# Kernel tuning notes

Measured on AMD Instinct MI355X. Metric: run time of the kernel, lower is better.

Reference implementation:

```python
import jax, jax.numpy as jnp
import numpy as np


def _ccl(x, w, b):
    # FFT-domain circular conv: rfft2 -> complex multiply + sum over c_in -> irfft2 + bias
    H, W = x.shape[-2], x.shape[-1]
    xf = jnp.fft.rfft2(x)                 # [B, Ci, H, Wf] complex
    wf = jnp.fft.rfft2(w, s=(H, W))       # [Co, Ci, H, Wf] complex
    hf = jnp.einsum('bihw,oihw->bohw', xf, wf)
    return jnp.fft.irfft2(hf, s=(H, W)) + b[:, None, None]


def _maxpool(x, ph, pw):
    B, C, H, W = x.shape
    return x.reshape(B, C, H // ph, ph, W // pw, pw).max(axis=(3, 5))


def _upsample_zero(x, sh, sw):
    B, C, H, W = x.shape
    y = jnp.zeros((B, C, H * sh, W * sw), dtype=x.dtype)
    return y.at[:, :, ::sh, ::sw].set(x)


def setup_inputs() -> dict:
    key = jax.random.key(0)
    ks = jax.random.split(key, 11)
    inp = {"x": jax.random.normal(ks[0], (16, 2, 64, 256), dtype=jnp.float32)}
    specs = [  # (c_out, c_in, kh, kw)
        (50, 1, 3, 7), (50, 50, 3, 7), (50, 50, 3, 5), (50, 50, 3, 7), (1, 50, 3, 7)]
    for i, (co, ci, kh, kw) in enumerate(specs):
        K = float(np.sqrt(1.0 / (ci * kh * kw)))
        inp[f"w{i+1}"] = (2 * jax.random.uniform(ks[2 * i + 1], (co, ci, kh, kw), dtype=jnp.float32) - 1) * K
        inp[f"b{i+1}"] = (2 * jax.random.uniform(ks[2 * i + 2], (co,), dtype=jnp.float32) - 1) * K
    return inp


def reference(x, w1, b1, w2, b2, w3, b3, w4, b4, w5, b5):
    H, W = x.shape[-2], x.shape[-1]
    h = x.reshape(-1, 1, H, W)                       # [2B, 1, 64, 256]
    h = jax.nn.relu(_maxpool(_ccl(h, w1, b1), 2, 4))  # [2B, 50, 32, 64]
    h = jax.nn.relu(_maxpool(_ccl(h, w2, b2), 2, 4))  # [2B, 50, 16, 16]
    h = h.reshape(-1, 2, h.shape[-3], h.shape[-2], h.shape[-1])
    h = h[:, 0] + h[:, 1].mean(axis=(-1, -2))[..., None, None]  # [B, 50, 16, 16]
    h = jax.nn.relu(_ccl(_upsample_zero(h, 2, 4), w3, b3))       # [B, 50, 32, 64]
    h = jax.nn.relu(_ccl(_upsample_zero(h, 2, 4), w4, b4))       # [B, 50, 64, 256]
    h = jax.nn.sigmoid(_ccl(h, w5, b5))                          # [B, 1, 64, 256]
    return h.squeeze(1)
```

## Files before the change

### kernel.cpp

```cpp
#include <hip/hip_runtime.h>
#include <math.h>

__global__ void kprep(const float* __restrict__ w2, const float* __restrict__ w3,
                      const float* __restrict__ w4, float* __restrict__ w2t,
                      float* __restrict__ w3t, float* __restrict__ w4t) {
  int i = blockIdx.x * 256 + threadIdx.x;
  if (i < 52500) {
    int co = i % 50, r = i / 50;
    w2t[i] = w2[co * 1050 + r];
    w4t[i] = w4[co * 1050 + r];
  } else {
    int j = i - 52500;
    if (j < 37500) {
      int co = j % 50, r = j / 50;
      w3t[j] = w3[co * 750 + r];
    }
  }
}

__global__ __launch_bounds__(256) void k1(const float* __restrict__ x,
                                          const float* __restrict__ w1,
                                          const float* __restrict__ b1,
                                          float* __restrict__ a1) {
  int b = blockIdx.z;
  int pr0 = blockIdx.x * 4;
  int co0 = blockIdx.y * 10;
  int ty = threadIdx.x >> 6;
  int pc = threadIdx.x & 63;
  int pr = pr0 + ty;
  const float* xb = x + b * (64 * 256);
  float xw[4][10];
#pragma unroll
  for (int r = 0; r < 4; ++r) {
    int row = (2 * pr - 2 + r) & 63;
#pragma unroll
    for (int c = 0; c < 10; ++c) {
      int col = (4 * pc - 6 + c) & 255;
      xw[r][c] = xb[row * 256 + col];
    }
  }
#pragma unroll
  for (int cq = 0; cq < 10; ++cq) {
    int co = co0 + cq;
    const float* wp = w1 + co * 21;
    float m = -1e30f;
#pragma unroll
    for (int iy = 0; iy < 2; ++iy) {
#pragma unroll
      for (int jx = 0; jx < 4; ++jx) {
        float s = 0.f;
#pragma unroll
        for (int di = 0; di < 3; ++di)
#pragma unroll
          for (int dj = 0; dj < 7; ++dj)
            s = fmaf(xw[iy + 2 - di][jx + 6 - dj], wp[di * 7 + dj], s);
        m = fmaxf(m, s);
      }
    }
    float v = fmaxf(m + b1[co], 0.f);
    a1[((b * 50 + co) * 32 + pr) * 64 + pc] = v;
  }
}

__global__ __launch_bounds__(256) void k2(const float* __restrict__ a1,
                                          const float* __restrict__ w2t,
                                          const float* __restrict__ b2,
                                          float* __restrict__ a2) {
  __shared__ float sm[3840];
  int b = blockIdx.z;
  int r0 = blockIdx.x * 4;
  int cc = blockIdx.y;
  int co0 = cc * 10;
  int y = threadIdx.x >> 6;
  int xcol = threadIdx.x & 63;
  float acc[10];
#pragma unroll
  for (int co = 0; co < 10; ++co) acc[co] = b2[co0 + co];
  const float* ain = a1 + b * (50 * 2048);
  for (int cci = 0; cci < 5; ++cci) {
    __syncthreads();
    for (int e = threadIdx.x; e < 3840; e += 256) {
      int ci = e / 384;
      int rr = (e >> 6) % 6;
      int col = e & 63;
      int row = (r0 - 2 + rr) & 31;
      sm[e] = ain[(cci * 10 + ci) * 2048 + row * 64 + col];
    }
    __syncthreads();
    for (int ci = 0; ci < 10; ++ci) {
      const float* sin_ = sm + ci * 384;
      const float* wbase = w2t + (cci * 10 + ci) * 21 * 50 + co0;
#pragma unroll
      for (int di = 0; di < 3; ++di) {
        const float* srow = sin_ + (y + 2 - di) * 64;
#pragma unroll
        for (int dj = 0; dj < 7; ++dj) {
          float xv = srow[(xcol - dj) & 63];
          const float* wrow = wbase + (di * 7 + dj) * 50;
#pragma unroll
          for (int co = 0; co < 10; ++co)
            acc[co] = fmaf(xv, wrow[co], acc[co]);
        }
      }
    }
  }
  __syncthreads();
#pragma unroll
  for (int k = 0; k < 10; ++k)
    sm[k * 256 + y * 64 + xcol] = acc[k];
  __syncthreads();
  for (int w = threadIdx.x; w < 320; w += 256) {
    int cop = w / 32;
    int pr = (w >> 4) & 1;
    int pc = w & 15;
    float m = -1e30f;
#pragma unroll
    for (int yy = 0; yy < 2; ++yy)
#pragma unroll
      for (int xx = 0; xx < 4; ++xx)
        m = fmaxf(m, sm[cop * 256 + (pr * 2 + yy) * 64 + pc * 4 + xx]);
    m = fmaxf(m, 0.f);
    a2[((b * 50 + co0 + cop) * 16 + (r0 >> 1) + pr) * 16 + pc] = m;
  }
}

__global__ __launch_bounds__(512) void k3(const float* __restrict__ a2,
                                          const float* __restrict__ w3t,
                                          const float* __restrict__ b3,
                                          float* __restrict__ a3) {
  __shared__ float ts[4000];
  __shared__ float mean_s[64];
  __shared__ float part[200];
  int b = blockIdx.z;
  int r0 = blockIdx.x * 8;
  int co0 = blockIdx.y * 10;
  int tid = threadIdx.x;
  const float* aodd = a2 + (2 * b + 1) * (50 * 256);
  if (tid < 200) {
    int ci = tid >> 2, p = tid & 3;
    float s = 0.f;
    for (int k = 0; k < 64; ++k) s += aodd[ci * 256 + p * 64 + k];
    part[tid] = s;
  }
  __syncthreads();
  if (tid < 50)
    mean_s[tid] = (part[4 * tid] + part[4 * tid + 1] + part[4 * tid + 2] + part[4 * tid + 3]) * (1.f / 256.f);
  __syncthreads();
  const float* aev = a2 + (2 * b) * (50 * 256);
  for (int e = tid; e < 4000; e += 512) {
    int ci = e / 80;
    int rr = (e >> 4) % 5;
    int tc = e & 15;
    int trow = ((r0 >> 1) - 1 + rr) & 15;
    ts[e] = aev[ci * 256 + trow * 16 + tc] + mean_s[ci];
  }
  __syncthreads();
  int wv = __builtin_amdgcn_readfirstlane(tid >> 6);
  int lane = tid & 63;
  int p = wv >> 2;
  int m = wv & 3;
  int q = lane & 15;
  int yidx = lane >> 4;
  int i = r0 + 2 * yidx + p;
  int j = 4 * q + m;
  float acc[10];
#pragma unroll
  for (int co = 0; co < 10; ++co) acc[co] = b3[co0 + co];
  int ndi = (p == 0) ? 2 : 1;
  int ndj = (m == 0) ? 2 : 1;
  for (int aa = 0; aa < ndi; ++aa) {
    int di = (p == 0) ? (2 * aa) : 1;
    int rr = 1 + ((2 * yidx + p - di) >> 1);
    for (int e2 = 0; e2 < ndj; ++e2) {
      int dj = (m == 0) ? (4 * e2) : m;
      int tc = ((j - dj + 64) >> 2) & 15;
      for (int ci = 0; ci < 50; ++ci) {
        float xv = ts[ci * 80 + rr * 16 + tc];
        const float* wrow = w3t + (ci * 15 + di * 5 + dj) * 50 + co0;
#pragma unroll
        for (int co = 0; co < 10; ++co)
          acc[co] = fmaf(xv, wrow[co], acc[co]);
      }
    }
  }
  float* aout = a3 + b * (50 * 2048);
#pragma unroll
  for (int co = 0; co < 10; ++co)
    aout[(co0 + co) * 2048 + i * 64 + j] = fmaxf(acc[co], 0.f);
}

__global__ __launch_bounds__(512) void k4(const float* __restrict__ a3,
                                          const float* __restrict__ w4t,
                                          const float* __restrict__ b4,
                                          float* __restrict__ a4) {
  __shared__ float s4[6400];
  int b = blockIdx.z;
  int r0 = blockIdx.x * 2;
  int co0 = blockIdx.y * 10;
  int tid = threadIdx.x;
  const float* ain = a3 + b * (50 * 2048);
  for (int e = tid; e < 6400; e += 512) {
    int ci = e >> 7;
    int rr = (e >> 6) & 1;
    int col = e & 63;
    int row = ((r0 >> 1) - 1 + rr) & 31;
    s4[e] = ain[ci * 2048 + row * 64 + col];
  }
  __syncthreads();
  int wv = __builtin_amdgcn_readfirstlane(tid >> 6);
  int lane = tid & 63;
  int rowsel = wv >> 2;
  int m = wv & 3;
  int i = r0 + rowsel;
  int j = 4 * lane + m;
  float acc[10];
#pragma unroll
  for (int co = 0; co < 10; ++co) acc[co] = b4[co0 + co];
  int ndi = (rowsel == 0) ? 2 : 1;
  int ndj = (m < 3) ? 2 : 1;
  for (int aa = 0; aa < ndi; ++aa) {
    int di = (rowsel == 0) ? (2 * aa) : 1;
    int rr = 1 - (di >> 1);
    for (int e2 = 0; e2 < ndj; ++e2) {
      int dj = m + 4 * e2;
      int tc = ((j - dj) >> 2) & 63;
      for (int ci = 0; ci < 50; ++ci) {
        float xv = s4[ci * 128 + rr * 64 + tc];
        const float* wrow = w4t + (ci * 21 + di * 7 + dj) * 50 + co0;
#pragma unroll
        for (int co = 0; co < 10; ++co)
          acc[co] = fmaf(xv, wrow[co], acc[co]);
      }
    }
  }
  float* aout = a4 + b * (50 * 16384);
#pragma unroll
  for (int co = 0; co < 10; ++co)
    aout[(co0 + co) * 16384 + i * 256 + j] = fmaxf(acc[co], 0.f);
}

__global__ __launch_bounds__(256) void k5(const float* __restrict__ a4,
                                          const float* __restrict__ w5,
                                          const float* __restrict__ b5,
                                          float* __restrict__ out) {
  __shared__ __align__(16) float s5[7920];
  int bid = blockIdx.x;
  int b = bid >> 4;
  int r0 = (bid & 15) * 4;
  int tid = threadIdx.x;
  int y = tid >> 6;
  int q = tid & 63;
  int j0 = q * 4;
  float acc0 = b5[0], acc1 = b5[0], acc2 = b5[0], acc3 = b5[0];
  const float* ain = a4 + b * (50 * 16384);
  for (int cc = 0; cc < 10; ++cc) {
    __syncthreads();
    for (int e = tid; e < 7920; e += 256) {
      int ci = e / 1584;
      int rr = (e / 264) % 6;
      int c = e % 264;
      int row = (r0 - 2 + rr) & 63;
      int col = (c - 8) & 255;
      s5[e] = ain[(cc * 5 + ci) * 16384 + row * 256 + col];
    }
    __syncthreads();
#pragma unroll
    for (int ci = 0; ci < 5; ++ci) {
#pragma unroll
      for (int di = 0; di < 3; ++di) {
        const float4* prow = (const float4*)&s5[ci * 1584 + (y + 2 - di) * 264 + j0];
        float4 v0 = prow[0], v1 = prow[1], v2 = prow[2];
        float wnd[12] = {v0.x, v0.y, v0.z, v0.w, v1.x, v1.y, v1.z, v1.w,
                         v2.x, v2.y, v2.z, v2.w};
        const float* wp = w5 + ((cc * 5 + ci) * 3 + di) * 7;
#pragma unroll
        for (int dj = 0; dj < 7; ++dj) {
          float wgt = wp[dj];
          acc0 = fmaf(wnd[8 - dj], wgt, acc0);
          acc1 = fmaf(wnd[9 - dj], wgt, acc1);
          acc2 = fmaf(wnd[10 - dj], wgt, acc2);
          acc3 = fmaf(wnd[11 - dj], wgt, acc3);
        }
      }
    }
  }
  float4 r;
  r.x = 1.f / (1.f + expf(-acc0));
  r.y = 1.f / (1.f + expf(-acc1));
  r.z = 1.f / (1.f + expf(-acc2));
  r.w = 1.f / (1.f + expf(-acc3));
  *(float4*)(out + b * 16384 + (r0 + y) * 256 + j0) = r;
}

extern "C" void kernel_launch(void* const* d_in, const int* in_sizes, int n_in,
                              void* d_out, int out_size, void* d_ws, size_t ws_size,
                              hipStream_t stream) {
  (void)in_sizes; (void)n_in; (void)out_size; (void)ws_size;
  const float* x  = (const float*)d_in[0];
  const float* w1 = (const float*)d_in[1];
  const float* b1 = (const float*)d_in[2];
  const float* w2 = (const float*)d_in[3];
  const float* b2 = (const float*)d_in[4];
  const float* w3 = (const float*)d_in[5];
  const float* b3 = (const float*)d_in[6];
  const float* w4 = (const float*)d_in[7];
  const float* b4 = (const float*)d_in[8];
  const float* w5 = (const float*)d_in[9];
  const float* b5 = (const float*)d_in[10];
  float* out = (float*)d_out;
  float* ws  = (float*)d_ws;
  float* w2t = ws;
  float* w3t = w2t + 52500;
  float* w4t = w3t + 37500;
  float* a1  = w4t + 52500;
  float* a2  = a1 + 32 * 50 * 32 * 64;
  float* a3  = a2 + 32 * 50 * 16 * 16;
  float* a4  = a3 + 16 * 50 * 32 * 64;
  hipLaunchKernelGGL(kprep, dim3(352), dim3(256), 0, stream, w2, w3, w4, w2t, w3t, w4t);
  hipLaunchKernelGGL(k1, dim3(8, 5, 32), dim3(256), 0, stream, x, w1, b1, a1);
  hipLaunchKernelGGL(k2, dim3(8, 5, 32), dim3(256), 0, stream, a1, w2t, b2, a2);
  hipLaunchKernelGGL(k3, dim3(4, 5, 16), dim3(512), 0, stream, a2, w3t, b3, a3);
  hipLaunchKernelGGL(k4, dim3(32, 5, 16), dim3(512), 0, stream, a3, w4t, b4, a4);
  hipLaunchKernelGGL(k5, dim3(256), dim3(256), 0, stream, a4, w5, b5, out);
}
```

Before: 368.6 us.

## Split output channels and input-channel ranges across more blocks with padded smem tiles

Halves per-block output channels in k1 and k3, and restructures k2 so each block computes two rows with waves split over channel halves. Shared-memory tiles in k2/k3/k4 gain halo padding so the inner loops use plain offsets instead of masked circular indexing. The final conv is split over five input-channel slices into partial buffers plus a reduction kernel that applies bias and sigmoid. This raises parallelism in the underfilled layers at the cost of more blocks, extra partial-sum traffic and an additional launch.

```diff
diff --git a/kernel.cpp b/kernel.cpp
--- a/kernel.cpp
+++ b/kernel.cpp
@@ -24,7 +24,7 @@
                                           float* __restrict__ a1) {
   int b = blockIdx.z;
   int pr0 = blockIdx.x * 4;
-  int co0 = blockIdx.y * 10;
+  int co0 = blockIdx.y * 5;
   int ty = threadIdx.x >> 6;
   int pc = threadIdx.x & 63;
   int pr = pr0 + ty;
@@ -40,7 +40,7 @@
     }
   }
 #pragma unroll
-  for (int cq = 0; cq < 10; ++cq) {
+  for (int cq = 0; cq < 5; ++cq) {
     int co = co0 + cq;
     const float* wp = w1 + co * 21;
     float m = -1e30f;
@@ -66,61 +66,63 @@
                                           const float* __restrict__ w2t,
                                           const float* __restrict__ b2,
                                           float* __restrict__ a2) {
-  __shared__ float sm[3840];
-  int b = blockIdx.z;
-  int r0 = blockIdx.x * 4;
-  int cc = blockIdx.y;
-  int co0 = cc * 10;
-  int y = threadIdx.x >> 6;
-  int xcol = threadIdx.x & 63;
-  float acc[10];
-#pragma unroll
-  for (int co = 0; co < 10; ++co) acc[co] = b2[co0 + co];
+  __shared__ float sm[2800];
+  int b = blockIdx.z;
+  int r0 = blockIdx.x * 2;
+  int co0 = blockIdx.y * 10;
+  int tid = threadIdx.x;
+  int lane = tid & 63;
+  int wv = tid >> 6;
+  int y = wv & 1;
+  int h = wv >> 1;
+  float acc[5];
+#pragma unroll
+  for (int c = 0; c < 5; ++c) acc[c] = b2[co0 + h * 5 + c];
   const float* ain = a1 + b * (50 * 2048);
   for (int cci = 0; cci < 5; ++cci) {
     __syncthreads();
-    for (int e = threadIdx.x; e < 3840; e += 256) {
-      int ci = e / 384;
-      int rr = (e >> 6) % 6;
-      int col = e & 63;
+    for (int e = tid; e < 2800; e += 256) {
+      int ci = e / 280;
+      int rem = e - ci * 280;
+      int rr = rem / 70;
+      int p = rem - rr * 70;
       int row = (r0 - 2 + rr) & 31;
+      int col = (p - 6) & 63;
       sm[e] = ain[(cci * 10 + ci) * 2048 + row * 64 + col];
     }
     __syncthreads();
     for (int ci = 0; ci < 10; ++ci) {
-      const float* sin_ = sm + ci * 384;
-      const float* wbase = w2t + (cci * 10 + ci) * 21 * 50 + co0;
+      const float* sp = sm + ci * 280 + y * 70 + lane;
+      const float* wp = w2t + (cci * 10 + ci) * 1050 + co0 + h * 5;
 #pragma unroll
       for (int di = 0; di < 3; ++di) {
-        const float* srow = sin_ + (y + 2 - di) * 64;
 #pragma unroll
         for (int dj = 0; dj < 7; ++dj) {
-          float xv = srow[(xcol - dj) & 63];
-          const float* wrow = wbase + (di * 7 + dj) * 50;
-#pragma unroll
-          for (int co = 0; co < 10; ++co)
-            acc[co] = fmaf(xv, wrow[co], acc[co]);
+          float xv = sp[(2 - di) * 70 + (6 - dj)];
+          const float* wrow = wp + (di * 7 + dj) * 50;
+#pragma unroll
+          for (int c = 0; c < 5; ++c)
+            acc[c] = fmaf(xv, wrow[c], acc[c]);
         }
       }
     }
   }
   __syncthreads();
 #pragma unroll
-  for (int k = 0; k < 10; ++k)
-    sm[k * 256 + y * 64 + xcol] = acc[k];
-  __syncthreads();
-  for (int w = threadIdx.x; w < 320; w += 256) {
-    int cop = w / 32;
-    int pr = (w >> 4) & 1;
-    int pc = w & 15;
+  for (int c = 0; c < 5; ++c)
+    sm[(h * 5 + c) * 128 + y * 64 + lane] = acc[c];
+  __syncthreads();
+  if (tid < 160) {
+    int co = tid >> 4;
+    int pc = tid & 15;
     float m = -1e30f;
 #pragma unroll
     for (int yy = 0; yy < 2; ++yy)
 #pragma unroll
       for (int xx = 0; xx < 4; ++xx)
-        m = fmaxf(m, sm[cop * 256 + (pr * 2 + yy) * 64 + pc * 4 + xx]);
+        m = fmaxf(m, sm[co * 128 + yy * 64 + pc * 4 + xx]);
     m = fmaxf(m, 0.f);
-    a2[((b * 50 + co0 + cop) * 16 + (r0 >> 1) + pr) * 16 + pc] = m;
+    a2[((b * 50 + co0 + co) * 16 + (r0 >> 1)) * 16 + pc] = m;
   }
 }
 
@@ -128,18 +130,18 @@
                                           const float* __restrict__ w3t,
                                           const float* __restrict__ b3,
                                           float* __restrict__ a3) {
-  __shared__ float ts[4000];
+  __shared__ float ts[4250];
   __shared__ float mean_s[64];
   __shared__ float part[200];
   int b = blockIdx.z;
   int r0 = blockIdx.x * 8;
-  int co0 = blockIdx.y * 10;
+  int co0 = blockIdx.y * 5;
   int tid = threadIdx.x;
   const float* aodd = a2 + (2 * b + 1) * (50 * 256);
   if (tid < 200) {
-    int ci = tid >> 2, p = tid & 3;
+    int ci = tid >> 2, pp = tid & 3;
     float s = 0.f;
-    for (int k = 0; k < 64; ++k) s += aodd[ci * 256 + p * 64 + k];
+    for (int k = 0; k < 64; ++k) s += aodd[ci * 256 + pp * 64 + k];
     part[tid] = s;
   }
   __syncthreads();
@@ -147,63 +149,68 @@
     mean_s[tid] = (part[4 * tid] + part[4 * tid + 1] + part[4 * tid + 2] + part[4 * tid + 3]) * (1.f / 256.f);
   __syncthreads();
   const float* aev = a2 + (2 * b) * (50 * 256);
-  for (int e = tid; e < 4000; e += 512) {
-    int ci = e / 80;
-    int rr = (e >> 4) % 5;
-    int tc = e & 15;
+  for (int e = tid; e < 4250; e += 512) {
+    int ci = e / 85;
+    int rem = e - ci * 85;
+    int rr = rem / 17;
+    int p = rem - rr * 17;
     int trow = ((r0 >> 1) - 1 + rr) & 15;
-    ts[e] = aev[ci * 256 + trow * 16 + tc] + mean_s[ci];
+    int col = (p - 1) & 15;
+    ts[e] = aev[ci * 256 + trow * 16 + col] + mean_s[ci];
   }
   __syncthreads();
   int wv = __builtin_amdgcn_readfirstlane(tid >> 6);
   int lane = tid & 63;
-  int p = wv >> 2;
+  int pcls = wv >> 2;
   int m = wv & 3;
   int q = lane & 15;
   int yidx = lane >> 4;
-  int i = r0 + 2 * yidx + p;
+  int i = r0 + 2 * yidx + pcls;
   int j = 4 * q + m;
-  float acc[10];
-#pragma unroll
-  for (int co = 0; co < 10; ++co) acc[co] = b3[co0 + co];
-  int ndi = (p == 0) ? 2 : 1;
+  float acc[5];
+#pragma unroll
+  for (int c = 0; c < 5; ++c) acc[c] = b3[co0 + c];
+  int ndi = (pcls == 0) ? 2 : 1;
   int ndj = (m == 0) ? 2 : 1;
-  for (int aa = 0; aa < ndi; ++aa) {
-    int di = (p == 0) ? (2 * aa) : 1;
-    int rr = 1 + ((2 * yidx + p - di) >> 1);
-    for (int e2 = 0; e2 < ndj; ++e2) {
-      int dj = (m == 0) ? (4 * e2) : m;
-      int tc = ((j - dj + 64) >> 2) & 15;
-      for (int ci = 0; ci < 50; ++ci) {
-        float xv = ts[ci * 80 + rr * 16 + tc];
-        const float* wrow = w3t + (ci * 15 + di * 5 + dj) * 50 + co0;
-#pragma unroll
-        for (int co = 0; co < 10; ++co)
-          acc[co] = fmaf(xv, wrow[co], acc[co]);
+  for (int ci = 0; ci < 50; ++ci) {
+    const float* sp = ts + ci * 85 + yidx * 17 + q;
+    const float* wp = w3t + ci * 750 + co0;
+    for (int aa = 0; aa < ndi; ++aa) {
+      int di = (pcls == 0) ? (2 * aa) : 1;
+      int rro = 1 - (di >> 1);
+      for (int e2 = 0; e2 < ndj; ++e2) {
+        int dj = (m == 0) ? (4 * e2) : m;
+        float xv = sp[rro * 17 + 1 - e2];
+        const float* wrow = wp + (di * 5 + dj) * 50;
+#pragma unroll
+        for (int c = 0; c < 5; ++c)
+          acc[c] = fmaf(xv, wrow[c], acc[c]);
       }
     }
   }
   float* aout = a3 + b * (50 * 2048);
 #pragma unroll
-  for (int co = 0; co < 10; ++co)
-    aout[(co0 + co) * 2048 + i * 64 + j] = fmaxf(acc[co], 0.f);
+  for (int c = 0; c < 5; ++c)
+    aout[(co0 + c) * 2048 + i * 64 + j] = fmaxf(acc[c], 0.f);
 }
 
 __global__ __launch_bounds__(512) void k4(const float* __restrict__ a3,
                                           const float* __restrict__ w4t,
                                           const float* __restrict__ b4,
                                           float* __restrict__ a4) {
-  __shared__ float s4[6400];
+  __shared__ float s4[6500];
   int b = blockIdx.z;
   int r0 = blockIdx.x * 2;
   int co0 = blockIdx.y * 10;
   int tid = threadIdx.x;
   const float* ain = a3 + b * (50 * 2048);
-  for (int e = tid; e < 6400; e += 512) {
-    int ci = e >> 7;
-    int rr = (e >> 6) & 1;
-    int col = e & 63;
+  for (int e = tid; e < 6500; e += 512) {
+    int ci = e / 130;
+    int rem = e - ci * 130;
+    int rr = rem / 65;
+    int p = rem - rr * 65;
     int row = ((r0 >> 1) - 1 + rr) & 31;
+    int col = (p - 1) & 63;
     s4[e] = ain[ci * 2048 + row * 64 + col];
   }
   __syncthreads();
@@ -218,15 +225,16 @@
   for (int co = 0; co < 10; ++co) acc[co] = b4[co0 + co];
   int ndi = (rowsel == 0) ? 2 : 1;
   int ndj = (m < 3) ? 2 : 1;
-  for (int aa = 0; aa < ndi; ++aa) {
-    int di = (rowsel == 0) ? (2 * aa) : 1;
-    int rr = 1 - (di >> 1);
-    for (int e2 = 0; e2 < ndj; ++e2) {
-      int dj = m + 4 * e2;
-      int tc = ((j - dj) >> 2) & 63;
-      for (int ci = 0; ci < 50; ++ci) {
-        float xv = s4[ci * 128 + rr * 64 + tc];
-        const float* wrow = w4t + (ci * 21 + di * 7 + dj) * 50 + co0;
+  for (int ci = 0; ci < 50; ++ci) {
+    const float* sp = s4 + ci * 130 + lane;
+    const float* wp = w4t + ci * 1050 + co0;
+    for (int aa = 0; aa < ndi; ++aa) {
+      int di = (rowsel == 0) ? (2 * aa) : 1;
+      int rro = 1 - (di >> 1);
+      for (int e2 = 0; e2 < ndj; ++e2) {
+        int dj = m + 4 * e2;
+        float xv = sp[rro * 65 + 1 - e2];
+        const float* wrow = wp + (di * 7 + dj) * 50;
 #pragma unroll
         for (int co = 0; co < 10; ++co)
           acc[co] = fmaf(xv, wrow[co], acc[co]);
@@ -239,21 +247,20 @@
     aout[(co0 + co) * 16384 + i * 256 + j] = fmaxf(acc[co], 0.f);
 }
 
-__global__ __launch_bounds__(256) void k5(const float* __restrict__ a4,
-                                          const float* __restrict__ w5,
-                                          const float* __restrict__ b5,
-                                          float* __restrict__ out) {
+__global__ __launch_bounds__(256) void k5a(const float* __restrict__ a4,
+                                           const float* __restrict__ w5,
+                                           float* __restrict__ p5) {
   __shared__ __align__(16) float s5[7920];
-  int bid = blockIdx.x;
-  int b = bid >> 4;
-  int r0 = (bid & 15) * 4;
+  int b = blockIdx.z;
+  int r0 = blockIdx.x * 4;
+  int cs = blockIdx.y;
   int tid = threadIdx.x;
   int y = tid >> 6;
   int q = tid & 63;
   int j0 = q * 4;
-  float acc0 = b5[0], acc1 = b5[0], acc2 = b5[0], acc3 = b5[0];
-  const float* ain = a4 + b * (50 * 16384);
-  for (int cc = 0; cc < 10; ++cc) {
+  float acc0 = 0.f, acc1 = 0.f, acc2 = 0.f, acc3 = 0.f;
+  const float* ain = a4 + b * (50 * 16384) + cs * 10 * 16384;
+  for (int cc = 0; cc < 2; ++cc) {
     __syncthreads();
     for (int e = tid; e < 7920; e += 256) {
       int ci = e / 1584;
@@ -272,7 +279,7 @@
         float4 v0 = prow[0], v1 = prow[1], v2 = prow[2];
         float wnd[12] = {v0.x, v0.y, v0.z, v0.w, v1.x, v1.y, v1.z, v1.w,
                          v2.x, v2.y, v2.z, v2.w};
-        const float* wp = w5 + ((cc * 5 + ci) * 3 + di) * 7;
+        const float* wp = w5 + ((cs * 10 + cc * 5 + ci) * 3 + di) * 7;
 #pragma unroll
         for (int dj = 0; dj < 7; ++dj) {
           float wgt = wp[dj];
@@ -284,12 +291,30 @@
       }
     }
   }
+  float4 r = {acc0, acc1, acc2, acc3};
+  *(float4*)(p5 + (cs * 16 + b) * 16384 + (r0 + y) * 256 + j0) = r;
+}
+
+__global__ __launch_bounds__(256) void k5b(const float* __restrict__ p5,
+                                           const float* __restrict__ b5,
+                                           float* __restrict__ out) {
+  int i = blockIdx.x * 256 + threadIdx.x;
+  int b = i >> 12;
+  int off = i & 4095;
+  const float4* p4 = (const float4*)p5;
+  float bias = b5[0];
+  float4 s = {bias, bias, bias, bias};
+#pragma unroll
+  for (int cs = 0; cs < 5; ++cs) {
+    float4 v = p4[(cs * 16 + b) * 4096 + off];
+    s.x += v.x; s.y += v.y; s.z += v.z; s.w += v.w;
+  }
   float4 r;
-  r.x = 1.f / (1.f + expf(-acc0));
-  r.y = 1.f / (1.f + expf(-acc1));
-  r.z = 1.f / (1.f + expf(-acc2));
-  r.w = 1.f / (1.f + expf(-acc3));
-  *(float4*)(out + b * 16384 + (r0 + y) * 256 + j0) = r;
+  r.x = 1.f / (1.f + expf(-s.x));
+  r.y = 1.f / (1.f + expf(-s.y));
+  r.z = 1.f / (1.f + expf(-s.z));
+  r.w = 1.f / (1.f + expf(-s.w));
+  ((float4*)out)[i] = r;
 }
 
 extern "C" void kernel_launch(void* const* d_in, const int* in_sizes, int n_in,
@@ -316,10 +341,12 @@
   float* a2  = a1 + 32 * 50 * 32 * 64;
   float* a3  = a2 + 32 * 50 * 16 * 16;
   float* a4  = a3 + 16 * 50 * 32 * 64;
+  float* p5  = a4 + 16 * 50 * 64 * 256;
   hipLaunchKernelGGL(kprep, dim3(352), dim3(256), 0, stream, w2, w3, w4, w2t, w3t, w4t);
-  hipLaunchKernelGGL(k1, dim3(8, 5, 32), dim3(256), 0, stream, x, w1, b1, a1);
-  hipLaunchKernelGGL(k2, dim3(8, 5, 32), dim3(256), 0, stream, a1, w2t, b2, a2);
-  hipLaunchKernelGGL(k3, dim3(4, 5, 16), dim3(512), 0, stream, a2, w3t, b3, a3);
+  hipLaunchKernelGGL(k1, dim3(8, 10, 32), dim3(256), 0, stream, x, w1, b1, a1);
+  hipLaunchKernelGGL(k2, dim3(16, 5, 32), dim3(256), 0, stream, a1, w2t, b2, a2);
+  hipLaunchKernelGGL(k3, dim3(4, 10, 16), dim3(512), 0, stream, a2, w3t, b3, a3);
   hipLaunchKernelGGL(k4, dim3(32, 5, 16), dim3(512), 0, stream, a3, w4t, b4, a4);
-  hipLaunchKernelGGL(k5, dim3(256), dim3(256), 0, stream, a4, w5, b5, out);
-}
+  hipLaunchKernelGGL(k5a, dim3(16, 5, 16), dim3(256), 0, stream, a4, w5, p5);
+  hipLaunchKernelGGL(k5b, dim3(256), dim3(256), 0, stream, p5, b5, out);
+}
```

After: 678.8 us. 1.84x slower.
